# Optimization experiments

Hardware: AMD Instinct MI355X
Metric: run time of the kernel (lower is better)

The kernel has to match this reference:

```python
import jax, jax.numpy as jnp
import numpy as np

N_NODES = 50000
N_EDGES = 600000
IN_DIM = 128
HID = 128
FEAT = 128
N_TASKS = 5
N_CLS = 10


def setup_inputs() -> dict:
    key = jax.random.key(0)
    ks = jax.random.split(key, 10)
    s = 0.05  # small init scale for weights
    return {
        "x": jax.random.normal(ks[0], (N_NODES, IN_DIM), jnp.float32),
        "edge_index": jax.random.randint(ks[1], (2, N_EDGES), 0, N_NODES, dtype=jnp.int32),
        "w1": jax.random.normal(ks[2], (IN_DIM, HID), jnp.float32) * s,
        "b1": jnp.zeros((HID,), jnp.float32),
        "w2": jax.random.normal(ks[3], (HID, HID), jnp.float32) * s,
        "b2": jnp.zeros((HID,), jnp.float32),
        "fw1": jax.random.normal(ks[4], (HID, FEAT), jnp.float32) * s,
        "fb1": jnp.zeros((FEAT,), jnp.float32),
        "fw2": jax.random.normal(ks[5], (FEAT, FEAT), jnp.float32) * s,
        "fb2": jnp.zeros((FEAT,), jnp.float32),
        "task_w": jax.random.normal(ks[6], (N_TASKS, FEAT, N_CLS), jnp.float32) * s,
        "task_b": jnp.zeros((N_TASKS, N_CLS), jnp.float32),
    }


def reference(x, edge_index, w1, b1, w2, b2, fw1, fb1, fw2, fb2, task_w, task_b):
    n = x.shape[0]
    # PyG GCNConv: add self-loops, symmetric D^{-1/2} A D^{-1/2} normalization.
    loop = jnp.arange(n, dtype=edge_index.dtype)
    src = jnp.concatenate([edge_index[0], loop])  # source nodes
    dst = jnp.concatenate([edge_index[1], loop])  # target (aggregation) nodes
    deg = jnp.zeros((n,), x.dtype).at[dst].add(jnp.ones((), x.dtype))
    dinv = jnp.where(deg > 0, jax.lax.rsqrt(deg), 0.0)
    norm = dinv[src] * dinv[dst]  # [E+N]

    def gcn_conv(h, w, b):
        h = h @ w                         # [N, H] linear transform
        msg = h[src] * norm[:, None]      # gather + normalize  [E+N, H]
        agg = jnp.zeros((n, h.shape[1]), h.dtype).at[dst].add(msg)  # scatter-add
        return agg + b

    h = jax.nn.relu(gcn_conv(x, w1, b1))
    # dropout(0.5) is identity at inference
    h = jax.nn.relu(gcn_conv(h, w2, b2))
    feature_x = jax.nn.relu(h @ fw1 + fb1)   # fc1
    h2 = jax.nn.relu(feature_x @ fw2 + fb2)  # fc2
    # per-task heads, all 128->10: batched as one einsum  [T, N, C]
    y = jnp.einsum('nf,tfc->tnc', h2, task_w) + task_b[:, None, :]
    return (y, feature_x)
```

## Files before the change

### kernel.cpp

```cpp
#include <hip/hip_runtime.h>
#include <hip/hip_bf16.h>

#define NN 50000
#define NE 600000
#define MM1_BLOCKS 1564
#define FILL_BLOCKS 2344
#define STRIDE 64

typedef __attribute__((ext_vector_type(4))) float f32x4;
typedef __attribute__((ext_vector_type(8))) __bf16 bf16x8;

__device__ __forceinline__ unsigned pack2bf16(float x, float y) {
  __bf16 lo = (__bf16)x, hi = (__bf16)y;
  unsigned short ul = __builtin_bit_cast(unsigned short, lo);
  unsigned short uh = __builtin_bit_cast(unsigned short, hi);
  return (unsigned)ul | ((unsigned)uh << 16);
}

__device__ __forceinline__ float lo16(unsigned v) { return __uint_as_float(v << 16); }
__device__ __forceinline__ float hi16(unsigned v) { return __uint_as_float(v & 0xffff0000u); }

__global__ void k_zero(int* __restrict__ cur) {
  int i = blockIdx.x * 256 + threadIdx.x;
  if (i < NN) cur[i] = 0;
}

__global__ void k_prep(const int* __restrict__ cur, int* __restrict__ degi,
                       float* __restrict__ dinv, int2* __restrict__ edg) {
  int n = blockIdx.x * 256 + threadIdx.x;
  if (n < NN) {
    int d = cur[n];
    degi[n] = d;
    dinv[n] = rsqrtf((float)(d + 1));
    int base = n * STRIDE;
    int pe = base + ((d + 7) & ~7);
    for (int j = base + d; j < pe; j++) edg[j] = make_int2(NN, NN);
  }
  if (n == 0) dinv[NN] = 0.f;
}

__device__ __forceinline__ void stage_wt64(const float* __restrict__ W, __bf16 (*wt)[136],
                                           int tid, int colbase) {
  int j = tid & 63;
  int kh = tid >> 6;
#pragma unroll
  for (int it = 0; it < 16; ++it) {
    int kp = ((it << 2) + kh + (j >> 3)) & 63;
    float w0 = W[(kp * 2) * 128 + colbase + j];
    float w1 = W[(kp * 2 + 1) * 128 + colbase + j];
    *(unsigned*)(&wt[j][kp * 2]) = pack2bf16(w0, w1);
  }
}

template<int BR, bool IN_BF16, bool DUAL>
__device__ __forceinline__ void mm_body64(const void* __restrict__ Xv, const __bf16 (*wt)[136],
                                          const float* __restrict__ bias, __bf16* __restrict__ Y,
                                          float* __restrict__ Yf, int strip, int lane, int colbase) {
  int r16 = lane & 15, g = lane >> 4;
  bf16x8 a[4];
  if constexpr (IN_BF16) {
    const __bf16* xb = (const __bf16*)Xv + (size_t)(strip * 16 + r16) * 128 + g * 8;
#pragma unroll
    for (int ks = 0; ks < 4; ks++) a[ks] = *(const bf16x8*)(xb + ks * 32);
  } else {
    const float* xb = (const float*)Xv + (size_t)(strip * 16 + r16) * 128 + g * 8;
#pragma unroll
    for (int ks = 0; ks < 4; ks++) {
      f32x4 x0 = *(const f32x4*)(xb + ks * 32);
      f32x4 x1 = *(const f32x4*)(xb + ks * 32 + 4);
      bf16x8 v;
      v[0] = (__bf16)x0.x; v[1] = (__bf16)x0.y; v[2] = (__bf16)x0.z; v[3] = (__bf16)x0.w;
      v[4] = (__bf16)x1.x; v[5] = (__bf16)x1.y; v[6] = (__bf16)x1.z; v[7] = (__bf16)x1.w;
      a[ks] = v;
    }
  }
  f32x4 acc[4];
#pragma unroll
  for (int ct = 0; ct < 4; ct++) acc[ct] = (f32x4){0.f, 0.f, 0.f, 0.f};
#pragma unroll
  for (int ct = 0; ct < 4; ct++) {
    const __bf16* wrow = &wt[ct * 16 + r16][g * 8];
#pragma unroll
    for (int ks = 0; ks < 4; ks++) {
      bf16x8 b = *(const bf16x8*)(wrow + ks * 32);
      acc[ct] = __builtin_amdgcn_mfma_f32_16x16x32_bf16(a[ks], b, acc[ct], 0, 0, 0);
    }
  }
  int rbase = strip * 16 + g * 4;
#pragma unroll
  for (int ct = 0; ct < 4; ct++) {
    int col = colbase + ct * 16 + r16;
    float bv = (BR & 1) ? bias[col] : 0.f;
#pragma unroll
    for (int i = 0; i < 4; i++) {
      float v = acc[ct][i] + bv;
      if (BR & 2) v = fmaxf(v, 0.f);
      size_t idx = (size_t)(rbase + i) * 128 + col;
      Y[idx] = (__bf16)v;
      if constexpr (DUAL) Yf[idx] = v;
    }
  }
}

template<int BR, bool IN_BF16, bool DUAL>
__global__ __launch_bounds__(256) void k_mm64(const void* __restrict__ Xv, const float* __restrict__ W,
                                              const float* __restrict__ bias, __bf16* __restrict__ Y,
                                              float* __restrict__ Yf, int nrows) {
  __shared__ __bf16 wt[64][136];
  int tid = threadIdx.x;
  int colbase = (blockIdx.x & 1) << 6;
  stage_wt64(W, wt, tid, colbase);
  __syncthreads();
  int strip = (blockIdx.x >> 1) * 4 + (tid >> 6);
  if (strip * 16 >= nrows) return;
  mm_body64<BR, IN_BF16, DUAL>(Xv, wt, bias, Y, Yf, strip, tid & 63, colbase);
}

__global__ __launch_bounds__(256) void k_mm1_fill(const float* __restrict__ X, const float* __restrict__ W,
                                                  __bf16* __restrict__ Y,
                                                  const int* __restrict__ srcv, const int* __restrict__ dstv,
                                                  int* __restrict__ cur, int2* __restrict__ edg) {
  __shared__ __bf16 wt[64][136];
  int tid = threadIdx.x;
  if (blockIdx.x >= MM1_BLOCKS) {
    int e = (blockIdx.x - MM1_BLOCKS) * 256 + tid;
    if (e < NE) {
      int s = srcv[e], d = dstv[e];
      int p = d * STRIDE + atomicAdd(&cur[d], 1);
      edg[p] = make_int2(s, s);
    }
    return;
  }
  int colbase = (blockIdx.x & 1) << 6;
  stage_wt64(W, wt, tid, colbase);
  __syncthreads();
  int strip = (blockIdx.x >> 1) * 4 + (tid >> 6);
  if (strip * 16 >= NN) return;
  mm_body64<0, false, false>(X, wt, nullptr, Y, nullptr, strip, tid & 63, colbase);
}

__global__ __launch_bounds__(256) void k_head(const __bf16* __restrict__ H, const float* __restrict__ TW,
                                              const float* __restrict__ TB, float* __restrict__ Y) {
  __shared__ __bf16 wt[64][136];
  int tid = threadIdx.x;
#pragma unroll
  for (int it = 0; it < 32; it++) {
    int i = it * 256 + tid;
    int o = i >> 7, k = i & 127;
    float v = (o < 50) ? TW[(o / 10) * 1280 + k * 10 + (o % 10)] : 0.f;
    wt[o][k] = (__bf16)v;
  }
  __syncthreads();
  int lane = tid & 63;
  int strip = blockIdx.x * 4 + (tid >> 6);
  if (strip * 16 >= NN) return;
  int r16 = lane & 15, g = lane >> 4;
  const __bf16* xb = H + (size_t)(strip * 16 + r16) * 128 + g * 8;
  bf16x8 a[4];
#pragma unroll
  for (int ks = 0; ks < 4; ks++) a[ks] = *(const bf16x8*)(xb + ks * 32);
  f32x4 acc[4];
#pragma unroll
  for (int ct = 0; ct < 4; ct++) acc[ct] = (f32x4){0.f, 0.f, 0.f, 0.f};
#pragma unroll
  for (int ct = 0; ct < 4; ct++) {
    const __bf16* wrow = &wt[ct * 16 + r16][g * 8];
#pragma unroll
    for (int ks = 0; ks < 4; ks++) {
      bf16x8 b = *(const bf16x8*)(wrow + ks * 32);
      acc[ct] = __builtin_amdgcn_mfma_f32_16x16x32_bf16(a[ks], b, acc[ct], 0, 0, 0);
    }
  }
  int rbase = strip * 16 + g * 4;
#pragma unroll
  for (int ct = 0; ct < 4; ct++) {
    int o = ct * 16 + r16;
    if (o < 50) {
      int t = o / 10, c = o % 10;
      float tb = TB[o];
#pragma unroll
      for (int i = 0; i < 4; i++) {
        Y[(size_t)t * (NN * 10) + (size_t)(rbase + i) * 10 + c] = acc[ct][i] + tb;
      }
    }
  }
}

__device__ __forceinline__ void edge8(const int2* __restrict__ edg, int i, const unsigned* __restrict__ T,
                                      const float* __restrict__ dinv, float dn,
                                      int lane, float& ax, float& ay) {
  const int4* ep = (const int4*)(edg + i);
  int4 p0 = ep[0], p1 = ep[1], p2 = ep[2], p3 = ep[3];
  int s0 = p0.x, s1 = p0.z, s2 = p1.x, s3 = p1.z;
  int s4 = p2.x, s5 = p2.z, s6 = p3.x, s7 = p3.z;
  float w0 = dinv[s0], w1 = dinv[s1], w2 = dinv[s2], w3 = dinv[s3];
  float w4 = dinv[s4], w5 = dinv[s5], w6 = dinv[s6], w7 = dinv[s7];
  unsigned v0 = T[s0 * 64 + lane];
  unsigned v1 = T[s1 * 64 + lane];
  unsigned v2 = T[s2 * 64 + lane];
  unsigned v3 = T[s3 * 64 + lane];
  unsigned v4 = T[s4 * 64 + lane];
  unsigned v5 = T[s5 * 64 + lane];
  unsigned v6 = T[s6 * 64 + lane];
  unsigned v7 = T[s7 * 64 + lane];
  w0 *= dn; w1 *= dn; w2 *= dn; w3 *= dn;
  w4 *= dn; w5 *= dn; w6 *= dn; w7 *= dn;
  ax = fmaf(lo16(v0), w0, ax); ay = fmaf(hi16(v0), w0, ay);
  ax = fmaf(lo16(v1), w1, ax); ay = fmaf(hi16(v1), w1, ay);
  ax = fmaf(lo16(v2), w2, ax); ay = fmaf(hi16(v2), w2, ay);
  ax = fmaf(lo16(v3), w3, ax); ay = fmaf(hi16(v3), w3, ay);
  ax = fmaf(lo16(v4), w4, ax); ay = fmaf(hi16(v4), w4, ay);
  ax = fmaf(lo16(v5), w5, ax); ay = fmaf(hi16(v5), w5, ay);
  ax = fmaf(lo16(v6), w6, ax); ay = fmaf(hi16(v6), w6, ay);
  ax = fmaf(lo16(v7), w7, ax); ay = fmaf(hi16(v7), w7, ay);
}

__global__ __launch_bounds__(256) void k_agg(const unsigned* __restrict__ T, const int* __restrict__ degi,
                                             const int2* __restrict__ edg, const float* __restrict__ dinv,
                                             const float* __restrict__ bias, unsigned* __restrict__ H) {
  int pair = blockIdx.x * 4 + (threadIdx.x >> 6);
  int nA = pair * 2, nB = nA + 1;
  int lane = threadIdx.x & 63;
  float2 b = ((const float2*)bias)[lane];
  float diA = dinv[nA], diB = dinv[nB];
  unsigned tA = T[(size_t)nA * 64 + lane];
  unsigned tB = T[(size_t)nB * 64 + lane];
  float axA = lo16(tA) * (diA * diA);
  float ayA = hi16(tA) * (diA * diA);
  float axB = lo16(tB) * (diB * diB);
  float ayB = hi16(tB) * (diB * diB);
  int iA = nA * STRIDE, eA = iA + ((degi[nA] + 7) & ~7);
  int iB = nB * STRIDE, eB = iB + ((degi[nB] + 7) & ~7);
  while (iA < eA && iB < eB) {
    edge8(edg, iA, T, dinv, diA, lane, axA, ayA);
    edge8(edg, iB, T, dinv, diB, lane, axB, ayB);
    iA += 8; iB += 8;
  }
  for (; iA < eA; iA += 8) edge8(edg, iA, T, dinv, diA, lane, axA, ayA);
  for (; iB < eB; iB += 8) edge8(edg, iB, T, dinv, diB, lane, axB, ayB);
  H[(size_t)nA * 64 + lane] = pack2bf16(fmaxf(axA + b.x, 0.f), fmaxf(ayA + b.y, 0.f));
  H[(size_t)nB * 64 + lane] = pack2bf16(fmaxf(axB + b.x, 0.f), fmaxf(ayB + b.y, 0.f));
}

extern "C" void kernel_launch(void* const* d_in, const int* in_sizes, int n_in,
                              void* d_out, int out_size, void* d_ws, size_t ws_size,
                              hipStream_t stream) {
  (void)in_sizes; (void)n_in; (void)out_size; (void)ws_size;
  const float* x   = (const float*)d_in[0];
  const int*   ei  = (const int*)d_in[1];
  const float* w1  = (const float*)d_in[2];
  const float* b1  = (const float*)d_in[3];
  const float* w2  = (const float*)d_in[4];
  const float* b2  = (const float*)d_in[5];
  const float* fw1 = (const float*)d_in[6];
  const float* fb1 = (const float*)d_in[7];
  const float* fw2 = (const float*)d_in[8];
  const float* fb2 = (const float*)d_in[9];
  const float* tw  = (const float*)d_in[10];
  const float* tb  = (const float*)d_in[11];
  const int* srcv = ei;
  const int* dstv = ei + NE;

  char* wsb = (char*)d_ws;
  __bf16* bufT = (__bf16*)(wsb + 0);
  __bf16* hbf  = (__bf16*)(wsb + 12800000);
  int*    degi = (int*)(wsb + 25600000);
  int*    cur  = (int*)(wsb + 25800000);
  float*  dinv = (float*)(wsb + 26000000);
  int2*   edg  = (int2*)(wsb + 26200064);

  float* y_out = (float*)d_out;
  float* feat  = (float*)d_out + 2500000;

  k_zero<<<196, 256, 0, stream>>>(cur);
  k_mm1_fill<<<MM1_BLOCKS + FILL_BLOCKS, 256, 0, stream>>>(x, w1, bufT, srcv, dstv, cur, edg);
  k_prep<<<196, 256, 0, stream>>>(cur, degi, dinv, edg);

  k_agg<<<6250, 256, 0, stream>>>((const unsigned*)bufT, degi, edg, dinv, b1, (unsigned*)hbf);
  k_mm64<0, true, false><<<1564, 256, 0, stream>>>(hbf, w2, nullptr, bufT, nullptr, NN);
  k_agg<<<6250, 256, 0, stream>>>((const unsigned*)bufT, degi, edg, dinv, b2, (unsigned*)hbf);
  k_mm64<3, true, true><<<1564, 256, 0, stream>>>(hbf, fw1, fb1, bufT, feat, NN);
  k_mm64<3, true, false><<<1564, 256, 0, stream>>>(bufT, fw2, fb2, hbf, nullptr, NN);
  k_head<<<782, 256, 0, stream>>>(hbf, tw, tb, y_out);
}
```

Measured before the change: 153.2 us.

## Fuse GCN aggregation with following dense matmul in one kernel

Merges the neighbor-aggregation kernel with the next 128x128 linear transform (w2, then fw1). Each block aggregates 8 nodes into shared memory and multiplies them by the staged weight matrix using bf16 MFMA. This removes two launches and one round trip of the hidden activations through global memory. In exchange every one of 6250 blocks restages the full 128x128 weight into LDS, wastes half the MFMA rows (8 real rows padded to 16), and writes outputs with scalar stores, all of which add redundant work.

```diff
diff --git a/kernel.cpp b/kernel.cpp
--- a/kernel.cpp
+++ b/kernel.cpp
@@ -215,13 +215,20 @@
   ax = fmaf(lo16(v7), w7, ax); ay = fmaf(hi16(v7), w7, ay);
 }
 
-__global__ __launch_bounds__(256) void k_agg(const unsigned* __restrict__ T, const int* __restrict__ degi,
-                                             const int2* __restrict__ edg, const float* __restrict__ dinv,
-                                             const float* __restrict__ bias, unsigned* __restrict__ H) {
-  int pair = blockIdx.x * 4 + (threadIdx.x >> 6);
-  int nA = pair * 2, nB = nA + 1;
-  int lane = threadIdx.x & 63;
-  float2 b = ((const float2*)bias)[lane];
+template<int BR, bool DUAL>
+__global__ __launch_bounds__(256) void k_aggmm(const unsigned* __restrict__ T, const int* __restrict__ degi,
+                                               const int2* __restrict__ edg, const float* __restrict__ dinv,
+                                               const float* __restrict__ bias_agg,
+                                               const float* __restrict__ W, const float* __restrict__ bias_mm,
+                                               __bf16* __restrict__ Y, float* __restrict__ Yf) {
+  __shared__ __bf16 wt[64][136];
+  __shared__ __bf16 stg[16][136];
+  int tid = threadIdx.x;
+  int lane = tid & 63, wv = tid >> 6;
+  unsigned* stgz = (unsigned*)&stg[8][0];
+  for (int i = tid; i < 544; i += 256) stgz[i] = 0u;
+  int nA = blockIdx.x * 8 + wv * 2, nB = nA + 1;
+  float2 b = ((const float2*)bias_agg)[lane];
   float diA = dinv[nA], diB = dinv[nB];
   unsigned tA = T[(size_t)nA * 64 + lane];
   unsigned tB = T[(size_t)nB * 64 + lane];
@@ -238,8 +245,38 @@
   }
   for (; iA < eA; iA += 8) edge8(edg, iA, T, dinv, diA, lane, axA, ayA);
   for (; iB < eB; iB += 8) edge8(edg, iB, T, dinv, diB, lane, axB, ayB);
-  H[(size_t)nA * 64 + lane] = pack2bf16(fmaxf(axA + b.x, 0.f), fmaxf(ayA + b.y, 0.f));
-  H[(size_t)nB * 64 + lane] = pack2bf16(fmaxf(axB + b.x, 0.f), fmaxf(ayB + b.y, 0.f));
+  unsigned* stgu = (unsigned*)stg;
+  stgu[(wv * 2) * 68 + lane] = pack2bf16(fmaxf(axA + b.x, 0.f), fmaxf(ayA + b.y, 0.f));
+  stgu[(wv * 2 + 1) * 68 + lane] = pack2bf16(fmaxf(axB + b.x, 0.f), fmaxf(ayB + b.y, 0.f));
+  __syncthreads();
+  int r16 = lane & 15, g = lane >> 4;
+  bf16x8 a[4];
+#pragma unroll
+  for (int ks = 0; ks < 4; ks++) a[ks] = *(const bf16x8*)(&stg[r16][g * 8 + ks * 32]);
+  int nodeBase = blockIdx.x * 8;
+#pragma unroll
+  for (int half = 0; half < 2; half++) {
+    stage_wt64(W, wt, tid, half * 64);
+    __syncthreads();
+    f32x4 acc = (f32x4){0.f, 0.f, 0.f, 0.f};
+    const __bf16* wrow = &wt[wv * 16 + r16][g * 8];
+#pragma unroll
+    for (int ks = 0; ks < 4; ks++)
+      acc = __builtin_amdgcn_mfma_f32_16x16x32_bf16(a[ks], *(const bf16x8*)(wrow + ks * 32), acc, 0, 0, 0);
+    if (g < 2) {
+      int col = half * 64 + wv * 16 + r16;
+      float bv = (BR & 1) ? bias_mm[col] : 0.f;
+#pragma unroll
+      for (int i = 0; i < 4; i++) {
+        float v = acc[i] + bv;
+        if (BR & 2) v = fmaxf(v, 0.f);
+        size_t idx = (size_t)(nodeBase + g * 4 + i) * 128 + col;
+        Y[idx] = (__bf16)v;
+        if constexpr (DUAL) Yf[idx] = v;
+      }
+    }
+    __syncthreads();
+  }
 }
 
 extern "C" void kernel_launch(void* const* d_in, const int* in_sizes, int n_in,
@@ -276,10 +313,10 @@
   k_mm1_fill<<<MM1_BLOCKS + FILL_BLOCKS, 256, 0, stream>>>(x, w1, bufT, srcv, dstv, cur, edg);
   k_prep<<<196, 256, 0, stream>>>(cur, degi, dinv, edg);
 
-  k_agg<<<6250, 256, 0, stream>>>((const unsigned*)bufT, degi, edg, dinv, b1, (unsigned*)hbf);
-  k_mm64<0, true, false><<<1564, 256, 0, stream>>>(hbf, w2, nullptr, bufT, nullptr, NN);
-  k_agg<<<6250, 256, 0, stream>>>((const unsigned*)bufT, degi, edg, dinv, b2, (unsigned*)hbf);
-  k_mm64<3, true, true><<<1564, 256, 0, stream>>>(hbf, fw1, fb1, bufT, feat, NN);
+  k_aggmm<0, false><<<6250, 256, 0, stream>>>((const unsigned*)bufT, degi, edg, dinv, b1,
+                                              w2, nullptr, hbf, nullptr);
+  k_aggmm<3, true><<<6250, 256, 0, stream>>>((const unsigned*)hbf, degi, edg, dinv, b2,
+                                             fw1, fb1, bufT, feat);
   k_mm64<3, true, false><<<1564, 256, 0, stream>>>(bufT, fw2, fb2, hbf, nullptr, NN);
   k_head<<<782, 256, 0, stream>>>(hbf, tw, tb, y_out);
 }
```

Result: slower. 174.2 us (+13.7%).
